# Performance work log

Measured on AMD Instinct MI355X. Metric: run time of the kernel, lower is better.

## Reference

```python
import jax, jax.numpy as jnp
import numpy as np

D = 384            # d_model
NUM_CLUSTERS = 100
MOM = 0.95         # cluster EMA momentum
ALPHA = 0.02 * (64.0 / D) ** 0.5  # SemanticMemoryLatentSpace alpha schedule
B = 512            # number of items processed sequentially
NORM_CAP = 50.0    # Frobenius-norm saturation threshold


def setup_inputs() -> dict:
    key = jax.random.key(0)
    k1, k2 = jax.random.split(key)
    embeddings = jax.random.normal(k1, (B, D), dtype=jnp.float32)
    # AdaptiveMemoryKernel init: L = randn*0.1 ; K0 = L L^T + 0.1 I (SPD-ish)
    L = jax.random.normal(k2, (D, D), dtype=jnp.float32) * 0.1
    kernel_init = L @ L.T + 0.1 * jnp.eye(D, dtype=jnp.float32)
    return {"embeddings": embeddings, "kernel_init": kernel_init}


def _forward(embeddings, kernel_init):
    def step(carry, e):
        K, prev_norm, count, C, cnts, active = carry
        # --- SemanticNoveltyTracker.compute_novelty: cosine sim vs active centroids ---
        e_norm = jnp.linalg.norm(e)
        c_norms = jnp.linalg.norm(C, axis=1)              # [num_clusters]
        sims = (C @ e) / (c_norms * e_norm + 1e-8)        # vectorized cosine sims
        mask = jnp.arange(NUM_CLUSTERS) < active
        sims_m = jnp.where(mask, sims, -2.0)              # mask inactive clusters
        max_sim = jnp.max(sims_m)
        closest = jnp.argmax(sims_m)
        novelty = jnp.where(active == 0, 1.0, 1.0 - max_sim ** 2)
        novelty = jnp.clip(novelty, 0.0, 1.0)
        # --- AdaptiveMemoryKernel.update_kernel ---
        pert = jnp.outer(e, e)                            # symmetric by construction
        tr = jnp.trace(pert)
        pert = jnp.where(tr > 1e-8, pert / jnp.maximum(tr, 1e-8) * D, pert)
        iw = novelty ** 1.5                               # squared-novelty weighting
        norm_before = jnp.linalg.norm(K)
        growth = jnp.where((count > 0) & (prev_norm > 0),
                           (norm_before - prev_norm) / jnp.maximum(prev_norm, 1e-12), 0.0)
        a = jnp.where(growth < 0.01, ALPHA * 1.5, ALPHA)  # boost when plateauing
        K = K + (a * iw) * pert
        K = (K + K.T) * 0.5                               # symmetrize
        kn = jnp.linalg.norm(K)
        K = jnp.where(kn > NORM_CAP, K / kn * NORM_CAP, K)  # soft saturation clip
        new_norm = jnp.linalg.norm(K)
        # --- SemanticNoveltyTracker.update_cluster ---
        create_new = (novelty > 0.7) & (active < NUM_CLUSTERS)
        idx = jnp.where(create_new, active, closest).astype(jnp.int32)
        old = C[idx]
        newc = jnp.where(create_new, e, MOM * old + (1.0 - MOM) * e)
        C = C.at[idx].set(newc)
        cnts = cnts.at[idx].set(jnp.where(create_new, 1.0, cnts[idx] + 1.0))
        active = active + create_new.astype(jnp.int32)
        return (K, new_norm, count + 1, C, cnts, active), None

    C0 = jnp.zeros((NUM_CLUSTERS, D), dtype=embeddings.dtype)
    cnts0 = jnp.zeros((NUM_CLUSTERS,), dtype=embeddings.dtype)
    init = (kernel_init, jnp.float32(0.0), jnp.int32(0), C0, cnts0, jnp.int32(0))
    (K, _, _, _, _, _), _ = jax.lax.scan(step, init, embeddings)
    # space warping: apply evolved kernel to the batch
    refined = embeddings @ K                              # [B, D]
    return refined


def reference(embeddings, kernel_init):
    return _forward(embeddings, kernel_init)
```

## Files before the change

kernel.cpp:

```cpp
#include <hip/hip_runtime.h>


#define A_BOOSTF 0.012247448713915891f

template <int CTRL>
__device__ __forceinline__ float dpp_f(float x) {
  return __int_as_float(
      __builtin_amdgcn_mov_dpp(__float_as_int(x), CTRL, 0xf, 0xf, true));
}
template <int CTRL>
__device__ __forceinline__ unsigned dpp_u(unsigned x) {
  return (unsigned)__builtin_amdgcn_mov_dpp((int)x, CTRL, 0xf, 0xf, true);
}
__device__ __forceinline__ float rdlane_f(float x, int l) {
  return __int_as_float(__builtin_amdgcn_readlane(__float_as_int(x), l));
}
__device__ __forceinline__ unsigned rdlane_u(unsigned x, int l) {
  return (unsigned)__builtin_amdgcn_readlane((int)x, l);
}
__device__ __forceinline__ float wave_sum64(float v) {
  v += dpp_f<0xB1>(v);
  v += dpp_f<0x4E>(v);
  v += dpp_f<0x124>(v);
  v += dpp_f<0x128>(v);
  return (rdlane_f(v, 0) + rdlane_f(v, 16)) + (rdlane_f(v, 32) + rdlane_f(v, 48));
}
__device__ __forceinline__ unsigned sortable(float v) {
  unsigned u = __float_as_uint(v);
  return u ^ (unsigned)(((int)u >> 31) | 0x80000000);
}
__device__ __forceinline__ float unsortable(unsigned x) {
  unsigned u = (x & 0x80000000u) ? (x ^ 0x80000000u) : ~x;
  return __uint_as_float(u);
}
__device__ __forceinline__ unsigned wave_umax64(unsigned v) {
  v = max(v, dpp_u<0xB1>(v));
  v = max(v, dpp_u<0x4E>(v));
  v = max(v, dpp_u<0x124>(v));
  v = max(v, dpp_u<0x128>(v));
  return max(max(rdlane_u(v, 0), rdlane_u(v, 16)),
             max(rdlane_u(v, 32), rdlane_u(v, 48)));
}

#define GX(D)                                                                  \
  ((D) < 4 ? ((D) == 0   ? gq[0].x                                             \
              : (D) == 1 ? gq[0].y                                             \
              : (D) == 2 ? gq[0].z                                             \
                         : gq[0].w)                                            \
   : (D) < 8                                                                   \
       ? ((D) == 4   ? gq[1].x                                                 \
          : (D) == 5 ? gq[1].y                                                 \
          : (D) == 6 ? gq[1].z                                                 \
                     : gq[1].w)                                                \
   : (D) < 12 ? ((D) == 8    ? gq[2].x                                         \
                 : (D) == 9  ? gq[2].y                                         \
                 : (D) == 10 ? gq[2].z                                         \
                             : gq[2].w)                                        \
              : ((D) == 12   ? gq[3].x                                         \
                 : (D) == 13 ? gq[3].y                                         \
                 : (D) == 14 ? gq[3].z                                         \
                             : gq[3].w))

__global__ __launch_bounds__(256) void gemm_nt(const float* __restrict__ A,
                                               const float* __restrict__ B,
                                               float* __restrict__ C,
                                               int N, int K) {
  __shared__ float As[32][33];
  __shared__ float Bs[32][33];
  int bx = blockIdx.x, by = blockIdx.y;
  int tid = threadIdx.x;
  int tx = tid & 15, ty = tid >> 4;
  float a00 = 0.f, a01 = 0.f, a10 = 0.f, a11 = 0.f;
  for (int k0 = 0; k0 < K; k0 += 32) {
    for (int l = tid; l < 1024; l += 256) {
      int r = l >> 5, c = l & 31;
      As[r][c] = A[(by * 32 + r) * K + k0 + c];
      Bs[r][c] = B[(bx * 32 + r) * K + k0 + c];
    }
    __syncthreads();
#pragma unroll
    for (int k = 0; k < 32; ++k) {
      float x0 = As[2 * ty][k], x1 = As[2 * ty + 1][k];
      float y0 = Bs[2 * tx][k], y1 = Bs[2 * tx + 1][k];
      a00 += x0 * y0; a01 += x0 * y1; a10 += x1 * y0; a11 += x1 * y1;
    }
    __syncthreads();
  }
  int i = by * 32 + 2 * ty, jj = bx * 32 + 2 * tx;
  C[i * N + jj] = a00;           C[i * N + jj + 1] = a01;
  C[(i + 1) * N + jj] = a10;     C[(i + 1) * N + jj + 1] = a11;
}

__global__ __launch_bounds__(256) void gemm_nn(const float* __restrict__ A,
                                               const float* __restrict__ B,
                                               float* __restrict__ C,
                                               int N, int K) {
  __shared__ float As[32][33];
  __shared__ float Bs[32][33];
  int bx = blockIdx.x, by = blockIdx.y;
  int tid = threadIdx.x;
  int tx = tid & 15, ty = tid >> 4;
  float a00 = 0.f, a01 = 0.f, a10 = 0.f, a11 = 0.f;
  for (int k0 = 0; k0 < K; k0 += 32) {
    for (int l = tid; l < 1024; l += 256) {
      int r = l >> 5, c = l & 31;
      As[r][c] = A[(by * 32 + r) * K + k0 + c];
      Bs[r][c] = B[(k0 + r) * N + bx * 32 + c];
    }
    __syncthreads();
#pragma unroll
    for (int k = 0; k < 32; ++k) {
      float x0 = As[2 * ty][k], x1 = As[2 * ty + 1][k];
      float y0 = Bs[k][2 * tx], y1 = Bs[k][2 * tx + 1];
      a00 += x0 * y0; a01 += x0 * y1; a10 += x1 * y0; a11 += x1 * y1;
    }
    __syncthreads();
  }
  int i = by * 32 + 2 * ty, jj = bx * 32 + 2 * tx;
  C[i * N + jj] = a00;           C[i * N + jj + 1] = a01;
  C[(i + 1) * N + jj] = a10;     C[(i + 1) * N + jj + 1] = a11;
}

__global__ __launch_bounds__(256) void final_gemm(const float* __restrict__ G,
                                                  const float* __restrict__ E,
                                                  const float* __restrict__ M0,
                                                  const float* __restrict__ W,
                                                  const float* __restrict__ gS,
                                                  float* __restrict__ out) {
  __shared__ float As[32][33];
  __shared__ float Bs[32][33];
  int bx = blockIdx.x, by = blockIdx.y;
  int tid = threadIdx.x;
  int tx = tid & 15, ty = tid >> 4;
  float a00 = 0.f, a01 = 0.f, a10 = 0.f, a11 = 0.f;
  for (int k0 = 0; k0 < 512; k0 += 32) {
    for (int l = tid; l < 1024; l += 256) {
      int r = l >> 5, c = l & 31;
      As[r][c] = G[(by * 32 + r) * 512 + k0 + c] * W[k0 + c];
      Bs[r][c] = E[(k0 + r) * 384 + bx * 32 + c];
    }
    __syncthreads();
#pragma unroll
    for (int k = 0; k < 32; ++k) {
      float x0 = As[2 * ty][k], x1 = As[2 * ty + 1][k];
      float y0 = Bs[k][2 * tx], y1 = Bs[k][2 * tx + 1];
      a00 += x0 * y0; a01 += x0 * y1; a10 += x1 * y0; a11 += x1 * y1;
    }
    __syncthreads();
  }
  float gv = gS[0];
  int i = by * 32 + 2 * ty, jj = bx * 32 + 2 * tx;
  out[i * 384 + jj]         = gv * M0[i * 384 + jj]         + a00;
  out[i * 384 + jj + 1]     = gv * M0[i * 384 + jj + 1]     + a01;
  out[(i + 1) * 384 + jj]     = gv * M0[(i + 1) * 384 + jj]     + a10;
  out[(i + 1) * 384 + jj + 1] = gv * M0[(i + 1) * 384 + jj + 1] + a11;
}

__global__ __launch_bounds__(256) void prep_kernel(const float* __restrict__ E,
                                                   const float* __restrict__ M0,
                                                   const float* __restrict__ K0,
                                                   float* __restrict__ u,
                                                   float* __restrict__ Kpart) {
  __shared__ double wr[4];
  int b = blockIdx.x;
  int tid = threadIdx.x, lane = tid & 63, wv = tid >> 6;
  if (b < 128) {
    int row = b * 4 + wv;
    const float4* e4 = (const float4*)(E + row * 384);
    const float4* m4 = (const float4*)(M0 + row * 384);
    float p = 0.f;
    for (int i = lane; i < 96; i += 64) {
      float4 a = e4[i], bb = m4[i];
      p += a.x * bb.x + a.y * bb.y + a.z * bb.z + a.w * bb.w;
    }
#pragma unroll
    for (int off = 32; off; off >>= 1) p += __shfl_down(p, off);
    if (lane == 0) u[row] = p;
  } else {
    int cb = b - 128;
    const float* p = K0 + cb * 2304 + tid * 9;
    double acc = 0.0;
#pragma unroll
    for (int i = 0; i < 9; ++i) { double v = (double)p[i]; acc += v * v; }
#pragma unroll
    for (int off = 32; off; off >>= 1) acc += __shfl_down(acc, off);
    if (lane == 0) wr[wv] = acc;
    __syncthreads();
    if (tid == 0) Kpart[cb] = (float)(wr[0] + wr[1] + wr[2] + wr[3]);
  }
}

__global__ __launch_bounds__(192) void scan_kernel(const float* __restrict__ G,
                                                   const float* __restrict__ u,
                                                   const float* __restrict__ Kpart,
                                                   float* __restrict__ Wout,
                                                   float* __restrict__ gOut) {
  __shared__ float RAW[100 * 257];
  __shared__ float gx_tbl[512 * 16];
  __shared__ float ren_tbl[512];
  __shared__ float u_sh[512];
  __shared__ float wh_sh[512];
  __shared__ float RG_bnew[512];
  __shared__ float RG_nov[512];
  __shared__ int RG_idx[512];
  __shared__ int FLAG;
  __shared__ int FLAG2;
  __shared__ int FLAG3A;
  __shared__ int FLAG3B;

  const int tid = threadIdx.x;
  const int wid = tid >> 6;
  const int lane = tid & 63;

  float4 z4 = {0.f, 0.f, 0.f, 0.f};
  for (int i = tid; i < 6425; i += 192) ((float4*)RAW)[i] = z4;
  for (int tt = tid; tt < 512; tt += 192) {
    const float* gr = G + tt * 512 + tt;
    const int lim = 512 - tt;
#pragma unroll
    for (int d = 0; d < 16; ++d)
      gx_tbl[tt * 16 + d] = (d < lim) ? gr[d] : 0.f;
    ren_tbl[tt] = __builtin_amdgcn_rcpf(__builtin_amdgcn_sqrtf(gr[0]));
  }
  if (tid < 128) ((float4*)u_sh)[tid] = ((const float4*)u)[tid];
  if (tid == 0) { FLAG = 0; FLAG2 = -1; FLAG3A = 0; FLAG3B = 0; }
  __syncthreads();

  if (wid == 0) {
    float d0 = 1.f, d1 = 1.f, cn0 = 0.f, cn1 = 0.f, s0 = 0.f, s1 = 0.f;
    int nact = 0;
    float r0[8], r1[8];
#pragma unroll
    for (int j = 0; j < 8; ++j) { r0[j] = 0.f; r1[j] = 0.f; }

    const float4* gx4 = (const float4*)gx_tbl;
    float4 gq[4];
    float renk;
    gq[0] = gx4[0]; gq[1] = gx4[1]; gq[2] = gx4[2]; gq[3] = gx4[3];
    renk = ren_tbl[0];

#define W0STEP(K)                                                              \
    {                                                                          \
      const int tnx = (t + (K) + 1 < 512) ? t + (K) + 1 : 511;                 \
      float4 gqn0 = gx4[tnx * 4], gqn1 = gx4[tnx * 4 + 1];                     \
      float4 gqn2 = gx4[tnx * 4 + 2], gqn3 = gx4[tnx * 4 + 3];                 \
      float renn = ren_tbl[tnx];                                               \
      const float trk = gq[0].x;                                               \
      float v0 = (lane < nact) ? s0 * renk * r0[K] : -2.f;                     \
      float v1 = (lane + 64 < nact) ? s1 * renk * r1[K] : -2.f;                \
      unsigned pk0 = (sortable(v0) & ~127u) | (unsigned)(127 - lane);          \
      unsigned pk1 = (sortable(v1) & ~127u) | (unsigned)(63 - lane);           \
      unsigned P = wave_umax64(max(pk0, pk1));                                 \
      int imax = 127 - (int)(P & 127u);                                        \
      float M = unsortable(P & ~127u);                                         \
      float nov = (nact == 0) ? 1.f : fminf(1.f, fmaxf(0.f, 1.f - M * M));     \
      int create = (nov > 0.7f && nact < 100) ? 1 : 0;                         \
      const int idxs = create ? nact : imax;                                   \
      const int cl = idxs & 63, hi = idxs >> 6;                                \
      float dcA = create ? 1.f : 0.95f * d0;                                   \
      float dcB = create ? 1.f : 0.95f * d1;                                   \
      float ccA = create ? trk                                                 \
                         : (0.9025f * cn0 + 0.095f * (d0 * r0[K]) +            \
                            0.0025f * trk);                                    \
      float ccB = create ? trk                                                 \
                         : (0.9025f * cn1 + 0.095f * (d1 * r1[K]) +            \
                            0.0025f * trk);                                    \
      float scA = dcA * __builtin_amdgcn_rcpf(__builtin_amdgcn_sqrtf(ccA));    \
      float scB = dcB * __builtin_amdgcn_rcpf(__builtin_amdgcn_sqrtf(ccB));    \
      float ivA = 0.05f * __builtin_amdgcn_rcpf(dcA);                          \
      float ivB = 0.05f * __builtin_amdgcn_rcpf(dcB);                          \
      bool own0 = (lane == cl) && (hi == 0);                                   \
      bool own1 = (lane == cl) && (hi == 1);                                   \
      d0 = own0 ? dcA : d0; cn0 = own0 ? ccA : cn0; s0 = own0 ? scA : s0;      \
      d1 = own1 ? dcB : d1; cn1 = own1 ? ccB : cn1; s1 = own1 ? scB : s1;      \
      float bnew = create ? 1.f : rdlane_f(hi ? ivB : ivA, cl);                \
      nact += create;                                                          \
      float pb0 = own0 ? bnew : 0.f, pb1 = own1 ? bnew : 0.f;                  \
      _Pragma("unroll") for (int j = (K) + 1; j < 8; ++j) {                    \
        r0[j] += pb0 * GX((j) - (K));                                          \
        r1[j] += pb1 * GX((j) - (K));                                          \
      }                                                                        \
      _Pragma("unroll") for (int j = 0; j < 8; ++j) {                          \
        pa0[j] += pb0 * GX(8 + (j) - (K));                                     \
        pa1[j] += pb1 * GX(8 + (j) - (K));                                     \
      }                                                                        \
      bnewA[K] = bnew; novA[K] = nov; idxA[K] = idxs;                          \
      gq[0] = gqn0; gq[1] = gqn1; gq[2] = gqn2; gq[3] = gqn3;                  \
      renk = renn;                                                             \
    }

    for (int R = 0; R < 64; ++R) {
      const int t = 8 * R;
      const int tn = t + 8;
      const int cnx = tn & 255;

      if (t == 256) {
        while (__hip_atomic_load(&FLAG3A, __ATOMIC_ACQUIRE,
                                 __HIP_MEMORY_SCOPE_WORKGROUP) == 0)
          __builtin_amdgcn_s_sleep(1);
        while (__hip_atomic_load(&FLAG3B, __ATOMIC_ACQUIRE,
                                 __HIP_MEMORY_SCOPE_WORKGROUP) == 0)
          __builtin_amdgcn_s_sleep(1);
#pragma unroll
        for (int j = 0; j < 8; ++j) r0[j] = RAW[lane * 257 + j];
        if (lane < 36) {
#pragma unroll
          for (int j = 0; j < 8; ++j) r1[j] = RAW[(lane + 64) * 257 + j];
        }
        __builtin_amdgcn_sched_barrier(0);
      }

      float bnewA[8], novA[8];
      int idxA[8];
      float pa0[8], pa1[8];
#pragma unroll
      for (int j = 0; j < 8; ++j) { pa0[j] = 0.f; pa1[j] = 0.f; }

      W0STEP(0) W0STEP(1) W0STEP(2) W0STEP(3)
      W0STEP(4) W0STEP(5) W0STEP(6) W0STEP(7)

      if (tn < 512 && cnx != 0) {
        while (__hip_atomic_load(&FLAG2, __ATOMIC_ACQUIRE,
                                 __HIP_MEMORY_SCOPE_WORKGROUP) < R - 1)
          __builtin_amdgcn_s_sleep(1);
        float r0n[8], r1n[8];
#pragma unroll
        for (int j = 0; j < 8; ++j) r0n[j] = RAW[lane * 257 + cnx + j];
        if (lane < 36) {
#pragma unroll
          for (int j = 0; j < 8; ++j) r1n[j] = RAW[(lane + 64) * 257 + cnx + j];
        } else {
#pragma unroll
          for (int j = 0; j < 8; ++j) r1n[j] = 0.f;
        }
#pragma unroll
        for (int j = 0; j < 8; ++j) {
          r0[j] = r0n[j] + pa0[j];
          r1[j] = r1n[j] + pa1[j];
        }
      }
      __builtin_amdgcn_sched_barrier(0);

      if (lane == 0) {
#pragma unroll
        for (int k = 0; k < 8; ++k) {
          RG_bnew[t + k] = bnewA[k];
          RG_nov[t + k] = novA[k];
          RG_idx[t + k] = idxA[k];
        }
        __hip_atomic_store(&FLAG, R + 1, __ATOMIC_RELEASE,
                           __HIP_MEMORY_SCOPE_WORKGROUP);
      }
    }
#undef W0STEP
  } else if (wid == 1) {
    for (int r = 0; r < 64; ++r) {
      const int t = 8 * r;
      const int c = t & 255;
      const int gbase = (t >> 6) & ~3;

      float B4[8][4];
#pragma unroll
      for (int k = 0; k < 8; ++k)
#pragma unroll
        for (int mg = 0; mg < 4; ++mg)
          B4[k][mg] = G[(t + k) * 512 + (gbase + mg) * 64 + lane];

      while (__hip_atomic_load(&FLAG, __ATOMIC_ACQUIRE,
                               __HIP_MEMORY_SCOPE_WORKGROUP) < r + 1)
        __builtin_amdgcn_s_sleep(1);

      float bn[8];
      int id[8];
#pragma unroll
      for (int k = 0; k < 8; ++k) { bn[k] = RG_bnew[t + k]; id[k] = RG_idx[t + k]; }

#pragma unroll
      for (int k = 0; k < 8; ++k) {
#pragma unroll
        for (int mg = 0; mg < 4; ++mg)
          if (mg * 64 + 63 >= c) {
            const int a_ = id[k] * 257 + mg * 64 + lane;
            RAW[a_] += bn[k] * B4[k][mg];
          }
      }
      __hip_atomic_store(&FLAG2, r, __ATOMIC_RELEASE,
                         __HIP_MEMORY_SCOPE_WORKGROUP);

      if (r == 31) {
        for (int i = lane; i < 3212; i += 64) ((float4*)RAW)[i] = z4;
        if (lane < 2) RAW[12848 + lane] = 0.f;
        __builtin_amdgcn_sched_barrier(0);
        const float* Gb = G + 256;
        for (int s = 0; s < 256; s += 4) {
          float A[4][4], bh[4];
          int idj[4];
#pragma unroll
          for (int j = 0; j < 4; ++j) {
            bh[j] = RG_bnew[s + j]; idj[j] = RG_idx[s + j];
#pragma unroll
            for (int m = 0; m < 4; ++m)
              A[j][m] = Gb[(s + j) * 512 + m * 64 + lane];
          }
#pragma unroll
          for (int j = 0; j < 4; ++j) {
            if (idj[j] < 50) {
#pragma unroll
              for (int m = 0; m < 4; ++m) {
                const int a_ = idj[j] * 257 + m * 64 + lane;
                RAW[a_] += bh[j] * A[j][m];
              }
            }
          }
        }
        __builtin_amdgcn_sched_barrier(0);
        __hip_atomic_store(&FLAG3A, 1, __ATOMIC_RELEASE,
                           __HIP_MEMORY_SCOPE_WORKGROUP);
      }
    }
  } else {
    float q8[8];
#pragma unroll
    for (int gI = 0; gI < 8; ++gI) q8[gI] = 0.f;
    float n2 = wave_sum64(Kpart[lane]);
    float g = 1.f, ginv = 1.f;

    for (int r = 0; r < 64; ++r) {
      const int t = 8 * r;

      if (r == 32) {
        while (__hip_atomic_load(&FLAG2, __ATOMIC_ACQUIRE,
                                 __HIP_MEMORY_SCOPE_WORKGROUP) < 31)
          __builtin_amdgcn_s_sleep(1);
        if (lane < 2) RAW[12850 + lane] = 0.f;
        for (int i = 3213 + lane; i < 6425; i += 64) ((float4*)RAW)[i] = z4;
        __builtin_amdgcn_sched_barrier(0);
        const float* Gb = G + 256;
        for (int s = 0; s < 256; s += 4) {
          float A[4][4], bh[4];
          int idj[4];
#pragma unroll
          for (int j = 0; j < 4; ++j) {
            bh[j] = RG_bnew[s + j]; idj[j] = RG_idx[s + j];
#pragma unroll
            for (int m = 0; m < 4; ++m)
              A[j][m] = Gb[(s + j) * 512 + m * 64 + lane];
          }
#pragma unroll
          for (int j = 0; j < 4; ++j) {
            if (idj[j] >= 50) {
#pragma unroll
              for (int m = 0; m < 4; ++m) {
                const int a_ = idj[j] * 257 + m * 64 + lane;
                RAW[a_] += bh[j] * A[j][m];
              }
            }
          }
        }
        __builtin_amdgcn_sched_barrier(0);
        __hip_atomic_store(&FLAG3B, 1, __ATOMIC_RELEASE,
                           __HIP_MEMORY_SCOPE_WORKGROUP);
      }

      float B[8][8];
#pragma unroll
      for (int k = 0; k < 8; ++k)
#pragma unroll
        for (int gI = 0; gI < 8; ++gI)
          B[k][gI] = G[(t + k) * 512 + gI * 64 + lane];

      while (__hip_atomic_load(&FLAG, __ATOMIC_ACQUIRE,
                               __HIP_MEMORY_SCOPE_WORKGROUP) < r + 1)
        __builtin_amdgcn_s_sleep(1);

      float novv[8];
#pragma unroll
      for (int k = 0; k < 8; ++k) novv[k] = RG_nov[t + k];

      float trm[8], gxw[8][8];
#pragma unroll
      for (int m = 0; m < 8; ++m) {
        trm[m] = gx_tbl[(t + m) * 16];
#pragma unroll
        for (int j = m + 1; j < 8; ++j)
          gxw[m][j] = gx_tbl[(t + m) * 16 + (j - m)];
      }
      float4 uuA = *(const float4*)&u_sh[t];
      float4 uuB = *(const float4*)&u_sh[t + 4];
      float um[8] = {uuA.x, uuA.y, uuA.z, uuA.w, uuB.x, uuB.y, uuB.z, uuB.w};

      const int grp = t >> 6;
      float qsel = q8[0];
#pragma unroll
      for (int gI = 1; gI < 8; ++gI) qsel = (grp == gI) ? q8[gI] : qsel;
      float qeff[8];
#pragma unroll
      for (int k = 0; k < 8; ++k) qeff[k] = rdlane_f(qsel, (t & 63) + k);

      float wh[8];
#pragma unroll
      for (int m = 0; m < 8; ++m) {
        float nov = novv[m];
        float iw = nov * __builtin_amdgcn_sqrtf(nov);
        float psc = 384.0f * __builtin_amdgcn_rcpf(fmaxf(trm[m], 1e-8f));
        float ccf = A_BOOSTF * iw * psc;
        float qv = g * (um[m] + qeff[m]);
        float n2n = n2 + 2.f * ccf * qv + ccf * ccf * trm[m] * trm[m];
        float kn = __builtin_amdgcn_sqrtf(n2n);
        float fct = (kn > 50.f) ? 50.f * __builtin_amdgcn_rcpf(kn) : 1.f;
        float fiv = (kn > 50.f) ? kn * 0.02f : 1.f;
        wh[m] = ccf * ginv;
        n2 = n2n * fct * fct; g *= fct; ginv *= fiv;
#pragma unroll
        for (int j = m + 1; j < 8; ++j)
          qeff[j] += wh[m] * gxw[m][j] * gxw[m][j];
      }

      if (lane == 0) {
#pragma unroll
        for (int m = 0; m < 8; ++m) wh_sh[t + m] = wh[m];
      }
#pragma unroll
      for (int gI = 0; gI < 8; ++gI)
#pragma unroll
        for (int k = 0; k < 8; ++k)
          q8[gI] += wh[k] * B[k][gI] * B[k][gI];
    }

    for (int s2 = lane; s2 < 512; s2 += 64) Wout[s2] = wh_sh[s2] * g;
    if (lane == 0) gOut[0] = g;
  }
}

extern "C" void kernel_launch(void* const* d_in, const int* in_sizes, int n_in,
                              void* d_out, int out_size, void* d_ws,
                              size_t ws_size, hipStream_t stream) {
  const float* E = (const float*)d_in[0];
  const float* K0 = (const float*)d_in[1];
  float* out = (float*)d_out;

  float* G = (float*)d_ws;
  float* M0 = G + 512 * 512;
  float* u = M0 + 512 * 384;
  float* W = u + 512;
  float* gS = W + 512;
  float* Kpart = gS + 1;

  gemm_nt<<<dim3(16, 16), 256, 0, stream>>>(E, E, G, 512, 384);
  gemm_nn<<<dim3(12, 16), 256, 0, stream>>>(E, K0, M0, 384, 384);
  prep_kernel<<<192, 256, 0, stream>>>(E, M0, K0, u, Kpart);
  scan_kernel<<<1, 192, 0, stream>>>(G, u, Kpart, W, gS);
  final_gemm<<<dim3(12, 16), 256, 0, stream>>>(G, E, M0, W, gS, out);
}
```

Before: 259.1 us.

## Fuse pre-scan GEMMs and norm reduction into one launch, compute u in scan

Merges the E·Eᵀ GEMM, the E·K0 GEMM and the K0 Frobenius-norm partials into a single kernel launch, dispatched by block index. The per-row dot product u = <E_i, M0_i> moves out of the prep kernel and into the single-block scan kernel's prologue, where each thread loops over rows serially. This removes two kernel launches and their inter-kernel gaps. In exchange the 512×384 dot products now run on one workgroup of 192 threads, which may lengthen the serial scan prologue.

```diff
diff --git a/kernel.cpp b/kernel.cpp
--- a/kernel.cpp
+++ b/kernel.cpp
@@ -61,64 +61,75 @@
                  : (D) == 14 ? gq[3].z                                         \
                              : gq[3].w))
 
-__global__ __launch_bounds__(256) void gemm_nt(const float* __restrict__ A,
-                                               const float* __restrict__ B,
-                                               float* __restrict__ C,
-                                               int N, int K) {
+__global__ __launch_bounds__(256) void fused_pre(const float* __restrict__ E,
+                                                 const float* __restrict__ K0,
+                                                 float* __restrict__ G,
+                                                 float* __restrict__ M0,
+                                                 float* __restrict__ Kpart) {
   __shared__ float As[32][33];
   __shared__ float Bs[32][33];
-  int bx = blockIdx.x, by = blockIdx.y;
-  int tid = threadIdx.x;
-  int tx = tid & 15, ty = tid >> 4;
-  float a00 = 0.f, a01 = 0.f, a10 = 0.f, a11 = 0.f;
-  for (int k0 = 0; k0 < K; k0 += 32) {
-    for (int l = tid; l < 1024; l += 256) {
-      int r = l >> 5, c = l & 31;
-      As[r][c] = A[(by * 32 + r) * K + k0 + c];
-      Bs[r][c] = B[(bx * 32 + r) * K + k0 + c];
-    }
+  const int b = blockIdx.x;
+  const int tid = threadIdx.x;
+
+  if (b < 256) {
+    const int bx = b & 15, by = b >> 4;
+    const int tx = tid & 15, ty = tid >> 4;
+    float a00 = 0.f, a01 = 0.f, a10 = 0.f, a11 = 0.f;
+    for (int k0 = 0; k0 < 384; k0 += 32) {
+      for (int l = tid; l < 1024; l += 256) {
+        int r = l >> 5, c = l & 31;
+        As[r][c] = E[(by * 32 + r) * 384 + k0 + c];
+        Bs[r][c] = E[(bx * 32 + r) * 384 + k0 + c];
+      }
+      __syncthreads();
+#pragma unroll
+      for (int k = 0; k < 32; ++k) {
+        float x0 = As[2 * ty][k], x1 = As[2 * ty + 1][k];
+        float y0 = Bs[2 * tx][k], y1 = Bs[2 * tx + 1][k];
+        a00 += x0 * y0; a01 += x0 * y1; a10 += x1 * y0; a11 += x1 * y1;
+      }
+      __syncthreads();
+    }
+    int i = by * 32 + 2 * ty, jj = bx * 32 + 2 * tx;
+    G[i * 512 + jj] = a00;           G[i * 512 + jj + 1] = a01;
+    G[(i + 1) * 512 + jj] = a10;     G[(i + 1) * 512 + jj + 1] = a11;
+  } else if (b < 448) {
+    const int bb = b - 256;
+    const int bx = bb % 12, by = bb / 12;
+    const int tx = tid & 15, ty = tid >> 4;
+    float a00 = 0.f, a01 = 0.f, a10 = 0.f, a11 = 0.f;
+    for (int k0 = 0; k0 < 384; k0 += 32) {
+      for (int l = tid; l < 1024; l += 256) {
+        int r = l >> 5, c = l & 31;
+        As[r][c] = E[(by * 32 + r) * 384 + k0 + c];
+        Bs[r][c] = K0[(k0 + r) * 384 + bx * 32 + c];
+      }
+      __syncthreads();
+#pragma unroll
+      for (int k = 0; k < 32; ++k) {
+        float x0 = As[2 * ty][k], x1 = As[2 * ty + 1][k];
+        float y0 = Bs[k][2 * tx], y1 = Bs[k][2 * tx + 1];
+        a00 += x0 * y0; a01 += x0 * y1; a10 += x1 * y0; a11 += x1 * y1;
+      }
+      __syncthreads();
+    }
+    int i = by * 32 + 2 * ty, jj = bx * 32 + 2 * tx;
+    M0[i * 384 + jj] = a00;           M0[i * 384 + jj + 1] = a01;
+    M0[(i + 1) * 384 + jj] = a10;     M0[(i + 1) * 384 + jj + 1] = a11;
+  } else {
+    __shared__ double wr[4];
+    const int cb = b - 448;
+    const int lane = tid & 63, wv = tid >> 6;
+    const float* p = K0 + cb * 2304 + tid * 9;
+    double acc = 0.0;
+#pragma unroll
+    for (int i = 0; i < 9; ++i) { double v = (double)p[i]; acc += v * v; }
+#pragma unroll
+    for (int off = 32; off; off >>= 1) acc += __shfl_down(acc, off);
+    if (lane == 0) wr[wv] = acc;
     __syncthreads();
-#pragma unroll
-    for (int k = 0; k < 32; ++k) {
-      float x0 = As[2 * ty][k], x1 = As[2 * ty + 1][k];
-      float y0 = Bs[2 * tx][k], y1 = Bs[2 * tx + 1][k];
-      a00 += x0 * y0; a01 += x0 * y1; a10 += x1 * y0; a11 += x1 * y1;
-    }
-    __syncthreads();
+    if (tid == 0) Kpart[cb] = (float)(wr[0] + wr[1] + wr[2] + wr[3]);
   }
-  int i = by * 32 + 2 * ty, jj = bx * 32 + 2 * tx;
-  C[i * N + jj] = a00;           C[i * N + jj + 1] = a01;
-  C[(i + 1) * N + jj] = a10;     C[(i + 1) * N + jj + 1] = a11;
-}
-
-__global__ __launch_bounds__(256) void gemm_nn(const float* __restrict__ A,
-                                               const float* __restrict__ B,
-                                               float* __restrict__ C,
-                                               int N, int K) {
-  __shared__ float As[32][33];
-  __shared__ float Bs[32][33];
-  int bx = blockIdx.x, by = blockIdx.y;
-  int tid = threadIdx.x;
-  int tx = tid & 15, ty = tid >> 4;
-  float a00 = 0.f, a01 = 0.f, a10 = 0.f, a11 = 0.f;
-  for (int k0 = 0; k0 < K; k0 += 32) {
-    for (int l = tid; l < 1024; l += 256) {
-      int r = l >> 5, c = l & 31;
-      As[r][c] = A[(by * 32 + r) * K + k0 + c];
-      Bs[r][c] = B[(k0 + r) * N + bx * 32 + c];
-    }
-    __syncthreads();
-#pragma unroll
-    for (int k = 0; k < 32; ++k) {
-      float x0 = As[2 * ty][k], x1 = As[2 * ty + 1][k];
-      float y0 = Bs[k][2 * tx], y1 = Bs[k][2 * tx + 1];
-      a00 += x0 * y0; a01 += x0 * y1; a10 += x1 * y0; a11 += x1 * y1;
-    }
-    __syncthreads();
-  }
-  int i = by * 32 + 2 * ty, jj = bx * 32 + 2 * tx;
-  C[i * N + jj] = a00;           C[i * N + jj + 1] = a01;
-  C[(i + 1) * N + jj] = a10;     C[(i + 1) * N + jj + 1] = a11;
 }
 
 __global__ __launch_bounds__(256) void final_gemm(const float* __restrict__ G,
@@ -156,42 +167,9 @@
   out[(i + 1) * 384 + jj + 1] = gv * M0[(i + 1) * 384 + jj + 1] + a11;
 }
 
-__global__ __launch_bounds__(256) void prep_kernel(const float* __restrict__ E,
+__global__ __launch_bounds__(192) void scan_kernel(const float* __restrict__ G,
+                                                   const float* __restrict__ E,
                                                    const float* __restrict__ M0,
-                                                   const float* __restrict__ K0,
-                                                   float* __restrict__ u,
-                                                   float* __restrict__ Kpart) {
-  __shared__ double wr[4];
-  int b = blockIdx.x;
-  int tid = threadIdx.x, lane = tid & 63, wv = tid >> 6;
-  if (b < 128) {
-    int row = b * 4 + wv;
-    const float4* e4 = (const float4*)(E + row * 384);
-    const float4* m4 = (const float4*)(M0 + row * 384);
-    float p = 0.f;
-    for (int i = lane; i < 96; i += 64) {
-      float4 a = e4[i], bb = m4[i];
-      p += a.x * bb.x + a.y * bb.y + a.z * bb.z + a.w * bb.w;
-    }
-#pragma unroll
-    for (int off = 32; off; off >>= 1) p += __shfl_down(p, off);
-    if (lane == 0) u[row] = p;
-  } else {
-    int cb = b - 128;
-    const float* p = K0 + cb * 2304 + tid * 9;
-    double acc = 0.0;
-#pragma unroll
-    for (int i = 0; i < 9; ++i) { double v = (double)p[i]; acc += v * v; }
-#pragma unroll
-    for (int off = 32; off; off >>= 1) acc += __shfl_down(acc, off);
-    if (lane == 0) wr[wv] = acc;
-    __syncthreads();
-    if (tid == 0) Kpart[cb] = (float)(wr[0] + wr[1] + wr[2] + wr[3]);
-  }
-}
-
-__global__ __launch_bounds__(192) void scan_kernel(const float* __restrict__ G,
-                                                   const float* __restrict__ u,
                                                    const float* __restrict__ Kpart,
                                                    float* __restrict__ Wout,
                                                    float* __restrict__ gOut) {
@@ -222,7 +200,17 @@
       gx_tbl[tt * 16 + d] = (d < lim) ? gr[d] : 0.f;
     ren_tbl[tt] = __builtin_amdgcn_rcpf(__builtin_amdgcn_sqrtf(gr[0]));
   }
-  if (tid < 128) ((float4*)u_sh)[tid] = ((const float4*)u)[tid];
+  for (int row = tid; row < 512; row += 192) {
+    const float4* m4 = (const float4*)(M0 + row * 384);
+    const float4* e4 = (const float4*)(E + row * 384);
+    float s = 0.f;
+#pragma unroll 4
+    for (int i = 0; i < 96; ++i) {
+      float4 a = m4[i], bb = e4[i];
+      s += a.x * bb.x + a.y * bb.y + a.z * bb.z + a.w * bb.w;
+    }
+    u_sh[row] = s;
+  }
   if (tid == 0) { FLAG = 0; FLAG2 = -1; FLAG3A = 0; FLAG3B = 0; }
   __syncthreads();
 
@@ -541,14 +529,11 @@
 
   float* G = (float*)d_ws;
   float* M0 = G + 512 * 512;
-  float* u = M0 + 512 * 384;
-  float* W = u + 512;
+  float* W = M0 + 512 * 384;
   float* gS = W + 512;
   float* Kpart = gS + 1;
 
-  gemm_nt<<<dim3(16, 16), 256, 0, stream>>>(E, E, G, 512, 384);
-  gemm_nn<<<dim3(12, 16), 256, 0, stream>>>(E, K0, M0, 384, 384);
-  prep_kernel<<<192, 256, 0, stream>>>(E, M0, K0, u, Kpart);
-  scan_kernel<<<1, 192, 0, stream>>>(G, u, Kpart, W, gS);
+  fused_pre<<<512, 256, 0, stream>>>(E, K0, G, M0, Kpart);
+  scan_kernel<<<1, 192, 0, stream>>>(G, E, M0, Kpart, W, gS);
   final_gemm<<<dim3(12, 16), 256, 0, stream>>>(G, E, M0, W, gS, out);
 }
```

After: 298.9 us. 1.15x slower.
